# Optimization experiments

Measured on AMD Instinct MI355X. Metric: run time of the kernel, lower is better.

The kernel has to match this reference:

```python
import jax, jax.numpy as jnp
import numpy as np

B, S, D = 2, 2048, 2560
H, HKV, HD = 8, 4, 256
EPS = 1e-6
SCALING = 256 ** -0.5          # query_pre_attn_scalar ** -0.5
SOFTCAP = 4096.0               # sliding_window passed positionally into softcap slot
NEG = -1e9


def rms_norm(x, w):
    # x: [..., HD]; computed in fp32 like the torch module
    xf = x.astype(jnp.float32)
    out = xf * jax.lax.rsqrt(jnp.mean(xf * xf, axis=-1, keepdims=True) + EPS)
    return (out * (1.0 + w.astype(jnp.float32))).astype(x.dtype)


def rotate_half(x):
    x1, x2 = x[..., : HD // 2], x[..., HD // 2:]
    return jnp.concatenate((-x2, x1), axis=-1)


def apply_rope(x, cos, sin):
    # cos/sin: [B, S, HD] -> broadcast over head axis 1
    c, s = cos[:, None], sin[:, None]
    return x * c + rotate_half(x) * s


def setup_inputs() -> dict:
    key = jax.random.key(0)
    ks = jax.random.split(key, 6)
    x = jax.random.normal(ks[0], (B, S, D), dtype=jnp.float32)
    # RoPE angles (theta=10000, linear scaling factor 8)
    inv_freq = 1.0 / (10000.0 ** (np.arange(0, HD, 2, dtype=np.float32) / HD))
    pos = np.arange(S, dtype=np.float32) / 8.0
    ang = np.einsum('s,d->sd', pos, inv_freq)
    ang = np.concatenate([ang, ang], axis=-1)               # [S, HD]
    cos = jnp.asarray(np.broadcast_to(np.cos(ang), (B, S, HD)).copy())
    sin = jnp.asarray(np.broadcast_to(np.sin(ang), (B, S, HD)).copy())
    # causal additive mask [B, 1, S, S]
    causal = np.where(np.tril(np.ones((S, S), dtype=bool)), 0.0, NEG).astype(np.float32)
    mask = jnp.asarray(np.broadcast_to(causal, (B, 1, S, S)).copy())
    sc = 0.02
    q_w = jax.random.normal(ks[1], (H * HD, D), dtype=jnp.float32) * sc
    k_w = jax.random.normal(ks[2], (HKV * HD, D), dtype=jnp.float32) * sc
    v_w = jax.random.normal(ks[3], (HKV * HD, D), dtype=jnp.float32) * sc
    o_w = jax.random.normal(ks[4], (D, H * HD), dtype=jnp.float32) * sc
    qn_w = jnp.zeros((HD,), dtype=jnp.float32)
    kn_w = jnp.zeros((HD,), dtype=jnp.float32)
    return {"x": x, "cos": cos, "sin": sin, "mask": mask,
            "q_w": q_w, "k_w": k_w, "v_w": v_w, "o_w": o_w,
            "qn_w": qn_w, "kn_w": kn_w}


def reference(x, cos, sin, mask, q_w, k_w, v_w, o_w, qn_w, kn_w):
    b, s, _ = x.shape
    # projections -> [B, H(kv), S, HD]
    q = (x @ q_w.T).reshape(b, s, H, HD).transpose(0, 2, 1, 3)
    k = (x @ k_w.T).reshape(b, s, HKV, HD).transpose(0, 2, 1, 3)
    v = (x @ v_w.T).reshape(b, s, HKV, HD).transpose(0, 2, 1, 3)
    q = rms_norm(q, qn_w)
    k = rms_norm(k, kn_w)
    q = apply_rope(q, cos, sin)
    k = apply_rope(k, cos, sin)
    # GQA: repeat kv heads (interleave matches repeat_interleave on dim=1)
    rep = H // HKV
    k = jnp.repeat(k, rep, axis=1)
    v = jnp.repeat(v, rep, axis=1)
    w = jnp.einsum('bhqd,bhkd->bhqk', q, k) * SCALING
    w = jnp.tanh(w / SOFTCAP) * SOFTCAP                     # softcap (bug-faithful)
    w = w + mask[:, :, :, : k.shape[2]]
    p = jax.nn.softmax(w.astype(jnp.float32), axis=-1).astype(q.dtype)
    attn = jnp.einsum('bhqk,bhkd->bhqd', p, v)
    attn = attn.transpose(0, 2, 1, 3).reshape(b, s, H * HD)
    return attn @ o_w.T
```

## Files before the change

### kernel.cpp

```cpp
#include <hip/hip_runtime.h>
#include <hip/hip_bf16.h>

#define BB   2
#define SS   2048
#define DD   2560
#define HH   8
#define HKVV 4
#define HDD  256
#define MM   (BB*SS)
#define NQ   (HH*HDD)
#define NKV  (HKVV*HDD)
#define SCALING 0.0625f
#define SOFTCAP 4096.0f
#define CAPC    (1.0f/(3.0f*SOFTCAP*SOFTCAP))
#define M0      20.0f

typedef __attribute__((ext_vector_type(8))) short short8;
typedef __attribute__((ext_vector_type(8))) unsigned short ushort8;
typedef __attribute__((ext_vector_type(4))) unsigned short us4;
typedef __attribute__((ext_vector_type(4))) float f32x4;

__device__ __forceinline__ float bf2f(unsigned short u) {
    union { unsigned int i; float f; } v; v.i = ((unsigned int)u) << 16; return v.f;
}
__device__ __forceinline__ unsigned short f2bf(float f) {
    union { float f; unsigned int i; } v; v.f = f;
    return (unsigned short)((v.i + 0x7fffu + ((v.i >> 16) & 1u)) >> 16);
}
__device__ __forceinline__ f32x4 mfma16(short8 a, short8 b, f32x4 c) {
    return __builtin_amdgcn_mfma_f32_16x16x32_bf16(a, b, c, 0, 0, 0);
}

__device__ __forceinline__ void async_cp16(const void* g, void* l) {
    __builtin_amdgcn_global_load_lds(
        (__attribute__((address_space(1))) void*)(g),
        (__attribute__((address_space(3))) void*)(l), 16, 0, 0);
}

__device__ __forceinline__ ushort8 ld8(const unsigned short* p) { return *(const ushort8*)p; }
__device__ __forceinline__ ushort8 ld8(const float* p) {
    ushort8 r;
#pragma unroll
    for (int i = 0; i < 8; i++) r[i] = f2bf(p[i]);
    return r;
}
__device__ __forceinline__ void stc(float* p, float v)          { *p = v; }
__device__ __forceinline__ void stc(unsigned short* p, float v) { *p = f2bf(v); }
__device__ __forceinline__ void stage8(const unsigned short* src, unsigned short* lds) {
    async_cp16(src, lds);
}
__device__ __forceinline__ void stage8(const float* src, unsigned short* lds) {
    *(ushort8*)lds = ld8(src);
}

__global__ __launch_bounds__(256) void cvt_bf16(const float* __restrict__ in,
                                                unsigned short* __restrict__ out, int n4)
{
    int i = blockIdx.x * 256 + threadIdx.x;
    const int stride = gridDim.x * 256;
    for (; i < n4; i += stride) {
        float4 v = ((const float4*)in)[i];
        us4 o;
        o[0] = f2bf(v.x); o[1] = f2bf(v.y); o[2] = f2bf(v.z); o[3] = f2bf(v.w);
        ((us4*)out)[i] = o;
    }
}

__global__ __launch_bounds__(256) void cvt_w4(const float* __restrict__ s0,
                                              const float* __restrict__ s1,
                                              const float* __restrict__ s2,
                                              const float* __restrict__ s3,
                                              unsigned short* __restrict__ dst)
{
    const int y = blockIdx.y;
    const int n4q = (int)((size_t)NQ  * DD / 4);
    const int n4k = (int)((size_t)NKV * DD / 4);
    const float* src; int n4; size_t off4;
    if (y == 0)      { src = s0; n4 = n4q; off4 = 0; }
    else if (y == 1) { src = s1; n4 = n4k; off4 = (size_t)n4q; }
    else if (y == 2) { src = s2; n4 = n4k; off4 = (size_t)n4q + n4k; }
    else             { src = s3; n4 = n4q; off4 = (size_t)n4q + 2 * (size_t)n4k; }
    us4* out = (us4*)dst + off4;
    int i = blockIdx.x * 256 + threadIdx.x;
    const int stride = gridDim.x * 256;
    for (; i < n4; i += stride) {
        float4 v = ((const float4*)src)[i];
        us4 o;
        o[0] = f2bf(v.x); o[1] = f2bf(v.y); o[2] = f2bf(v.z); o[3] = f2bf(v.w);
        out[i] = o;
    }
}

template<typename TA, typename TB, typename TC, bool VT_OUT>
__global__ __launch_bounds__(256) void gemm_k(const TA* __restrict__ A,
                                              const TB* __restrict__ Bm,
                                              TC* __restrict__ C,
                                              int M, int N, int K)
{
    __shared__ __align__(16) unsigned short As[128][32];
    __shared__ __align__(16) unsigned short Bs[128][32];

    const int tid  = threadIdx.x;
    const int bm   = blockIdx.x, bn = blockIdx.y;
    const int wave = tid >> 6, lane = tid & 63;
    const int quad = lane >> 4, lm = lane & 15;
    const int wm = (wave >> 1) * 64, wn = (wave & 1) * 64;

    f32x4 acc[4][4];
#pragma unroll
    for (int i = 0; i < 4; i++)
#pragma unroll
        for (int j = 0; j < 4; j++) acc[i][j] = (f32x4)0.0f;

    unsigned short* AsF = &As[0][0];
    unsigned short* BsF = &Bs[0][0];
    const int grow = tid >> 2;
    const int gcol = (tid & 3) * 8;
    const TA* Ab = A  + (size_t)(bm * 128) * K;
    const TB* Bb = Bm + (size_t)(bn * 128) * K;

    for (int k0 = 0; k0 < K; k0 += 32) {
        stage8(&Ab[(size_t)(grow     ) * K + k0 + gcol], AsF + tid * 8);
        stage8(&Ab[(size_t)(grow + 64) * K + k0 + gcol], AsF + 2048 + tid * 8);
        stage8(&Bb[(size_t)(grow     ) * K + k0 + gcol], BsF + tid * 8);
        stage8(&Bb[(size_t)(grow + 64) * K + k0 + gcol], BsF + 2048 + tid * 8);
        __syncthreads();

        short8 af[4], bf[4];
#pragma unroll
        for (int t = 0; t < 4; t++) af[t] = *(const short8*)&As[wm + t * 16 + lm][quad * 8];
#pragma unroll
        for (int t = 0; t < 4; t++) bf[t] = *(const short8*)&Bs[wn + t * 16 + lm][quad * 8];
#pragma unroll
        for (int i = 0; i < 4; i++)
#pragma unroll
            for (int j = 0; j < 4; j++)
                acc[i][j] = mfma16(af[i], bf[j], acc[i][j]);
        __syncthreads();
    }

#pragma unroll
    for (int i = 0; i < 4; i++)
#pragma unroll
        for (int j = 0; j < 4; j++) {
            if constexpr (VT_OUT) {
                int row0 = bm * 128 + wm + i * 16 + quad * 4;
                int col  = bn * 128 + wn + j * 16 + lm;
                int b    = row0 >> 11, s0 = row0 & (SS - 1);
                int kvh  = col >> 8,   d  = col & (HDD - 1);
                us4 pk;
#pragma unroll
                for (int r = 0; r < 4; r++) pk[r] = f2bf(acc[i][j][r]);
                *(us4*)&C[(((size_t)b * HKVV + kvh) * HDD + d) * SS + s0] = pk;
            } else {
#pragma unroll
                for (int r = 0; r < 4; r++) {
                    int row = bm * 128 + wm + i * 16 + quad * 4 + r;
                    int col = bn * 128 + wn + j * 16 + lm;
                    stc(&C[(size_t)row * N + col], acc[i][j][r]);
                }
            }
        }
}

__global__ __launch_bounds__(512, 2) void gemm_qkv256(const unsigned short* __restrict__ A,
                                                      const unsigned short* __restrict__ Bm,
                                                      unsigned short* __restrict__ Qo,
                                                      unsigned short* __restrict__ Ko,
                                                      unsigned short* __restrict__ Vo,
                                                      int K)
{
    __shared__ __align__(16) unsigned short Asm[2][256 * 64];
    __shared__ __align__(16) unsigned short Bsm[2][256 * 64];

    const int tid  = threadIdx.x;
    const int wid  = tid >> 6, lane = tid & 63;
    const int quad = lane >> 4, lm = lane & 15;
    const int wr   = wid >> 2, wc = wid & 3;
    const int bm   = blockIdx.x, bn = blockIdx.y;

    f32x4 acc[8][4];
#pragma unroll
    for (int i = 0; i < 8; i++)
#pragma unroll
        for (int j = 0; j < 4; j++) acc[i][j] = (f32x4)0.0f;

    const unsigned short* Ab = A  + (size_t)(bm * 256) * K;
    const unsigned short* Bb = Bm + (size_t)(bn * 256) * K;

    auto STAGE = [&](int buf, int k0) {
#pragma unroll
        for (int p = 0; p < 4; p++) {
            const int slot = p * 512 + tid;
            const int row = slot >> 3, ch = slot & 7;
            async_cp16(&Ab[(size_t)row * K + k0 + ((ch ^ (row & 7)) * 8)],
                       &Asm[buf][slot * 8]);
        }
#pragma unroll
        for (int p = 0; p < 4; p++) {
            const int slot = p * 512 + tid;
            const int row = slot >> 3, ch = slot & 7;
            async_cp16(&Bb[(size_t)row * K + k0 + ((ch ^ (row & 7)) * 8)],
                       &Bsm[buf][slot * 8]);
        }
    };

#define LOAD_A(MH)                                                                \
    _Pragma("unroll")                                                             \
    for (int mi = 0; mi < 4; mi++) {                                              \
        const int arow = wr * 128 + ((MH) * 4 + mi) * 16 + lm;                    \
        _Pragma("unroll")                                                         \
        for (int ks = 0; ks < 2; ks++)                                            \
            a_[mi][ks] = *(const short8*)&Asm[cur][arow * 64 +                    \
                            (((ks * 4 + quad) ^ (arow & 7)) * 8)];                \
    }
#define LOAD_B(NH)                                                                \
    _Pragma("unroll")                                                             \
    for (int ni = 0; ni < 2; ni++) {                                              \
        const int brow = wc * 64 + ((NH) * 2 + ni) * 16 + lm;                     \
        _Pragma("unroll")                                                         \
        for (int ks = 0; ks < 2; ks++)                                            \
            b_[ni][ks] = *(const short8*)&Bsm[cur][brow * 64 +                    \
                            (((ks * 4 + quad) ^ (brow & 7)) * 8)];                \
    }
#define MFMA_PH(MH, NH)                                                           \
    asm volatile("s_waitcnt lgkmcnt(0)" ::: "memory");                            \
    __builtin_amdgcn_sched_barrier(0);                                            \
    __builtin_amdgcn_s_setprio(1);                                                \
    _Pragma("unroll")                                                             \
    for (int mi = 0; mi < 4; mi++)                                                \
        _Pragma("unroll")                                                         \
        for (int ni = 0; ni < 2; ni++)                                            \
            _Pragma("unroll")                                                     \
            for (int ks = 0; ks < 2; ks++)                                        \
                acc[(MH) * 4 + mi][(NH) * 2 + ni] =                               \
                    mfma16(a_[mi][ks], b_[ni][ks],                                \
                           acc[(MH) * 4 + mi][(NH) * 2 + ni]);                    \
    __builtin_amdgcn_s_setprio(0);                                                \
    __builtin_amdgcn_sched_barrier(0);

    const int NT = K >> 6;
    STAGE(0, 0);
    int cur = 0;

    for (int t = 0; t < NT; t++) {
        if (t + 1 < NT) {
            STAGE(cur ^ 1, (t + 1) * 64);
            asm volatile("s_waitcnt vmcnt(8)" ::: "memory");
        } else {
            asm volatile("s_waitcnt vmcnt(0)" ::: "memory");
        }
        __builtin_amdgcn_s_barrier();
        __builtin_amdgcn_sched_barrier(0);

        short8 a_[4][2], b_[2][2];
        LOAD_A(0) LOAD_B(0) MFMA_PH(0, 0)
        LOAD_B(1)           MFMA_PH(0, 1)
        LOAD_A(1)           MFMA_PH(1, 1)
        LOAD_B(0)           MFMA_PH(1, 0)

        __builtin_amdgcn_s_barrier();
        __builtin_amdgcn_sched_barrier(0);
        cur ^= 1;
    }
#undef LOAD_A
#undef LOAD_B
#undef MFMA_PH

    if (bn < 8) {
#pragma unroll
        for (int m = 0; m < 8; m++)
#pragma unroll
            for (int n = 0; n < 4; n++) {
                const int row0 = bm * 256 + wr * 128 + m * 16 + quad * 4;
                const int colg = bn * 256 + wc * 64 + n * 16 + lm;
#pragma unroll
                for (int r = 0; r < 4; r++)
                    Qo[(size_t)(row0 + r) * NQ + colg] = f2bf(acc[m][n][r]);
            }
    } else if (bn < 12) {
#pragma unroll
        for (int m = 0; m < 8; m++)
#pragma unroll
            for (int n = 0; n < 4; n++) {
                const int row0 = bm * 256 + wr * 128 + m * 16 + quad * 4;
                const int ck   = bn * 256 + wc * 64 + n * 16 + lm - 2048;
#pragma unroll
                for (int r = 0; r < 4; r++)
                    Ko[(size_t)(row0 + r) * NKV + ck] = f2bf(acc[m][n][r]);
            }
    } else {
#pragma unroll
        for (int m = 0; m < 8; m++)
#pragma unroll
            for (int n = 0; n < 4; n++) {
                const int row0 = bm * 256 + wr * 128 + m * 16 + quad * 4;
                const int cv   = bn * 256 + wc * 64 + n * 16 + lm - 3072;
                const int b = row0 >> 11, s0 = row0 & (SS - 1);
                const int kvh = cv >> 8, d = cv & (HDD - 1);
                us4 pk;
#pragma unroll
                for (int r = 0; r < 4; r++) pk[r] = f2bf(acc[m][n][r]);
                *(us4*)&Vo[(((size_t)b * HKVV + kvh) * HDD + d) * SS + s0] = pk;
            }
    }
}

template<typename TA>
__global__ __launch_bounds__(256) void gemm_qkv(const TA* __restrict__ A,
                                                const unsigned short* __restrict__ Bm,
                                                unsigned short* __restrict__ Qo,
                                                unsigned short* __restrict__ Ko,
                                                unsigned short* __restrict__ Vo,
                                                int K)
{
    __shared__ __align__(16) unsigned short As[128][32];
    __shared__ __align__(16) unsigned short Bs[128][32];

    const int tid  = threadIdx.x;
    const int bm   = blockIdx.x, bn = blockIdx.y;
    const int wave = tid >> 6, lane = tid & 63;
    const int quad = lane >> 4, lm = lane & 15;
    const int wm = (wave >> 1) * 64, wn = (wave & 1) * 64;

    f32x4 acc[4][4];
#pragma unroll
    for (int i = 0; i < 4; i++)
#pragma unroll
        for (int j = 0; j < 4; j++) acc[i][j] = (f32x4)0.0f;

    unsigned short* AsF = &As[0][0];
    unsigned short* BsF = &Bs[0][0];
    const int grow = tid >> 2;
    const int gcol = (tid & 3) * 8;
    const TA* Ab = A  + (size_t)(bm * 128) * K;
    const unsigned short* Bb = Bm + (size_t)(bn * 128) * K;

    for (int k0 = 0; k0 < K; k0 += 32) {
        stage8(&Ab[(size_t)(grow     ) * K + k0 + gcol], AsF + tid * 8);
        stage8(&Ab[(size_t)(grow + 64) * K + k0 + gcol], AsF + 2048 + tid * 8);
        stage8(&Bb[(size_t)(grow     ) * K + k0 + gcol], BsF + tid * 8);
        stage8(&Bb[(size_t)(grow + 64) * K + k0 + gcol], BsF + 2048 + tid * 8);
        __syncthreads();

        short8 af[4], bf[4];
#pragma unroll
        for (int t = 0; t < 4; t++) af[t] = *(const short8*)&As[wm + t * 16 + lm][quad * 8];
#pragma unroll
        for (int t = 0; t < 4; t++) bf[t] = *(const short8*)&Bs[wn + t * 16 + lm][quad * 8];
#pragma unroll
        for (int i = 0; i < 4; i++)
#pragma unroll
            for (int j = 0; j < 4; j++)
                acc[i][j] = mfma16(af[i], bf[j], acc[i][j]);
        __syncthreads();
    }

#pragma unroll
    for (int i = 0; i < 4; i++)
#pragma unroll
        for (int j = 0; j < 4; j++) {
            const int row0 = bm * 128 + wm + i * 16 + quad * 4;
            const int col  = bn * 128 + wn + j * 16 + lm;
            if (col < 2048) {
#pragma unroll
                for (int r = 0; r < 4; r++)
                    Qo[(size_t)(row0 + r) * NQ + col] = f2bf(acc[i][j][r]);
            } else if (col < 3072) {
                const int ck = col - 2048;
#pragma unroll
                for (int r = 0; r < 4; r++)
                    Ko[(size_t)(row0 + r) * NKV + ck] = f2bf(acc[i][j][r]);
            } else {
                const int cv = col - 3072;
                const int b = row0 >> 11, s0 = row0 & (SS - 1);
                const int kvh = cv >> 8, d = cv & (HDD - 1);
                us4 pk;
#pragma unroll
                for (int r = 0; r < 4; r++) pk[r] = f2bf(acc[i][j][r]);
                *(us4*)&Vo[(((size_t)b * HKVV + kvh) * HDD + d) * SS + s0] = pk;
            }
        }
}

__global__ __launch_bounds__(256) void norm_rope2(unsigned short* __restrict__ Qx,
                                                  unsigned short* __restrict__ Kx,
                                                  const float* __restrict__ qnw,
                                                  const float* __restrict__ knw,
                                                  const float* __restrict__ cosb,
                                                  const float* __restrict__ sinb)
{
    const int bs = blockIdx.x;
    const int y  = blockIdx.y;
    const int t  = threadIdx.x;
    unsigned short* X; const float* nw; int nheads, h;
    if (y < HH) { X = Qx; nw = qnw; nheads = HH;   h = y; }
    else        { X = Kx; nw = knw; nheads = HKVV; h = y - HH; }

    __shared__ float xs[256];
    __shared__ float red[4];

    const size_t base = ((size_t)bs * nheads + h) * HDD;
    float v = bf2f(X[base + t]);
    xs[t] = v;

    float p = v * v;
#pragma unroll
    for (int off = 32; off >= 1; off >>= 1) p += __shfl_xor(p, off);
    if ((t & 63) == 0) red[t >> 6] = p;
    __syncthreads();
    float sum = red[0] + red[1] + red[2] + red[3];
    float rs  = rsqrtf(sum * (1.0f / HDD) + 1e-6f);

    const int pt = (t + 128) & 255;
    float w1 = 1.0f + nw[t];
    float w2 = 1.0f + nw[pt];
    float normed  = v * rs * w1;
    float partner = xs[pt] * rs * w2;
    float rot = (t < 128) ? -partner : partner;
    float c = cosb[(size_t)bs * HDD + t];
    float s = sinb[(size_t)bs * HDD + t];
    X[base + t] = f2bf(normed * c + rot * s);
}

__global__ __launch_bounds__(256) void norm_rope(unsigned short* __restrict__ X,
                                                 const float* __restrict__ nw,
                                                 const float* __restrict__ cosb,
                                                 const float* __restrict__ sinb,
                                                 int nheads)
{
    const int bs = blockIdx.x;
    const int h  = blockIdx.y;
    const int t  = threadIdx.x;

    __shared__ float xs[256];
    __shared__ float red[4];

    const size_t base = ((size_t)bs * nheads + h) * HDD;
    float v = bf2f(X[base + t]);
    xs[t] = v;

    float p = v * v;
#pragma unroll
    for (int off = 32; off >= 1; off >>= 1) p += __shfl_xor(p, off);
    if ((t & 63) == 0) red[t >> 6] = p;
    __syncthreads();
    float sum = red[0] + red[1] + red[2] + red[3];
    float rs  = rsqrtf(sum * (1.0f / HDD) + 1e-6f);

    const int pt = (t + 128) & 255;
    float w1 = 1.0f + nw[t];
    float w2 = 1.0f + nw[pt];
    float normed  = v * rs * w1;
    float partner = xs[pt] * rs * w2;
    float rot = (t < 128) ? -partner : partner;
    float c = cosb[(size_t)bs * HDD + t];
    float s = sinb[(size_t)bs * HDD + t];
    X[base + t] = f2bf(normed * c + rot * s);
}

__device__ const unsigned char unit_tbl[48] = {
    62, 124, 125, 120, 121,
    58, 116, 117, 112, 113,
    54, 108, 109, 104, 105,
    50, 100, 101,  96,  97,
    46,  92,  93,  88,  89,
    42,  84,  85,  80,  81,
    38,  76,  77,  72,  73,
    34,  68,  69,  64,  65,
    30,  26,  22,  18,  14, 10, 6, 2
};

__global__ __launch_bounds__(256) void attn_split(const unsigned short* __restrict__ Q,
                                                  const unsigned short* __restrict__ K,
                                                  const unsigned short* __restrict__ VT,
                                                  unsigned short* __restrict__ O,
                                                  float* __restrict__ Opart,
                                                  float* __restrict__ lpart)
{
    const int tid = threadIdx.x, w = tid >> 6, lane = tid & 63;
    const int quad = lane >> 4, lm = lane & 15;
    const int hb = blockIdx.x;
    const int h = hb & 7, b = hb >> 3, kvh = h >> 1;

    const unsigned int u = unit_tbl[blockIdx.y];
    const int qb = u >> 2;
    const bool single = (u & 2) != 0;
    const int half = u & 1;
    const int q0 = qb * 64;
    const int T  = 2 * (qb + 1);
    const int t_lo = (!single && half) ? (qb + 1) : 0;
    const int t_hi = single ? T : (half ? T : (qb + 1));

    __shared__ __align__(16) unsigned short Ks[2][32 * 256];
    __shared__ __align__(16) unsigned short Vt[256 * 32];
    __shared__ __align__(16) unsigned short Ps[4 * 512];

    const unsigned short* Qb = Q + (((size_t)b * SS + q0 + w * 16 + lm) * HH + h) * HDD;
    short8 qf[8];
#pragma unroll
    for (int c = 0; c < 8; c++) qf[c] = *(const short8*)&Qb[c * 32 + quad * 8];

    const unsigned short* Kb = K  + (size_t)b * SS * NKV + (size_t)kvh * HDD;
    const unsigned short* Vb = VT + ((size_t)b * HKVV + kvh) * HDD * (size_t)SS;

    f32x4 o_acc[16];
#pragma unroll
    for (int i = 0; i < 16; i++) o_acc[i] = (f32x4)0.0f;
    float l_r[4] = {0.f, 0.f, 0.f, 0.f};

    const int mylo = q0 + w * 16;
    const int row  = mylo + quad * 4;

    auto STAGE_K = [&](int bi, int k0) {
#pragma unroll
        for (int p = 0; p < 4; p++) {
            const int slot = p * 256 + tid;
            const int krow = slot >> 5, kc = slot & 31;
            async_cp16(&Kb[(size_t)(k0 + krow) * NKV + ((kc ^ (krow & 7)) * 8)],
                       &Ks[bi][slot * 8]);
        }
    };
    auto STAGE_V = [&](int k0) {
#pragma unroll
        for (int p = 0; p < 4; p++) {
            const int slot = p * 256 + tid;
            const int vd = slot >> 2, vc = slot & 3;
            async_cp16(&Vb[(size_t)vd * SS + k0 + ((vc ^ ((vd >> 1) & 3)) * 8)],
                       &Vt[slot * 8]);
        }
    };

    STAGE_K(0, t_lo * 32);
    STAGE_V(t_lo * 32);
    int cur = 0;

    for (int t = t_lo; t < t_hi; t++) {
        const int k0 = t * 32;
        const bool more = (t + 1 < t_hi);

        if (more) {
            STAGE_K(cur ^ 1, k0 + 32);
            asm volatile("s_waitcnt vmcnt(8)" ::: "memory");
        } else {
            asm volatile("s_waitcnt vmcnt(4)" ::: "memory");
        }
        __builtin_amdgcn_s_barrier();
        __builtin_amdgcn_sched_barrier(0);

        short8 pf;
        if (k0 <= mylo + 15) {
            f32x4 sa0 = (f32x4)0.0f, sa1 = (f32x4)0.0f;
            __builtin_amdgcn_s_setprio(1);
#pragma unroll
            for (int c = 0; c < 8; c++) {
                const int cs = (((c * 4 + quad) ^ (lm & 7))) * 8;
                short8 kf0 = *(const short8*)&Ks[cur][lm * 256 + cs];
                short8 kf1 = *(const short8*)&Ks[cur][(16 + lm) * 256 + cs];
                sa0 = mfma16(qf[c], kf0, sa0);
                sa1 = mfma16(qf[c], kf1, sa1);
            }
            __builtin_amdgcn_s_setprio(0);

            const bool msk = (k0 + 31 > mylo);
            float pe[2][4];
#pragma unroll
            for (int t2 = 0; t2 < 2; t2++) {
                const int key = k0 + t2 * 16 + lm;
#pragma unroll
                for (int r = 0; r < 4; r++) {
                    float s = (t2 ? sa1[r] : sa0[r]) * SCALING;
                    s = s - s * s * s * CAPC;
                    float e = __expf(s - M0);
                    if (msk && key > row + r) e = 0.0f;
                    pe[t2][r] = e;
                    l_r[r] += e;
                }
            }

#pragma unroll
            for (int t2 = 0; t2 < 2; t2++)
#pragma unroll
                for (int r = 0; r < 4; r++) {
                    const int g = (t2 * 2 + (lm >> 3)) ^ r ^ quad;
                    Ps[w * 512 + (quad * 4 + r) * 32 + g * 8 + (lm & 7)] = f2bf(pe[t2][r]);
                }
            asm volatile("s_waitcnt lgkmcnt(0)" ::: "memory");
            __builtin_amdgcn_sched_barrier(0);
            const int gr = quad ^ (lm & 3) ^ (lm >> 2);
            pf = *(const short8*)&Ps[w * 512 + lm * 32 + gr * 8];
        }

        if (more) asm volatile("s_waitcnt vmcnt(4)" ::: "memory");
        else      asm volatile("s_waitcnt vmcnt(0)" ::: "memory");
        __builtin_amdgcn_s_barrier();
        __builtin_amdgcn_sched_barrier(0);

        if (k0 <= mylo + 15) {
            __builtin_amdgcn_s_setprio(1);
#pragma unroll
            for (int nt = 0; nt < 16; nt++) {
                short8 vf = *(const short8*)&Vt[(nt * 16 + lm) * 32
                                                + ((quad ^ ((lm >> 1) & 3)) * 8)];
                o_acc[nt] = mfma16(pf, vf, o_acc[nt]);
            }
            __builtin_amdgcn_s_setprio(0);
        }

        __builtin_amdgcn_sched_barrier(0);
        __builtin_amdgcn_s_barrier();
        __builtin_amdgcn_sched_barrier(0);
        if (more) STAGE_V(k0 + 32);
        cur ^= 1;
    }

#pragma unroll
    for (int off = 1; off < 16; off <<= 1)
#pragma unroll
        for (int r = 0; r < 4; r++) l_r[r] += __shfl_xor(l_r[r], off);

    if (single) {
#pragma unroll
        for (int r = 0; r < 4; r++) {
            float inv = 1.0f / l_r[r];
            unsigned short* Ob = O + ((size_t)b * SS + row + r) * NQ + h * HDD;
#pragma unroll
            for (int nt = 0; nt < 16; nt++)
                Ob[nt * 16 + lm] = f2bf(o_acc[nt][r] * inv);
        }
    } else {
        const int slot = (((b * HH + h) * 16 + (qb - 16)) << 1) | half;
        float* Ob = Opart + ((size_t)slot * 64 + w * 16 + quad * 4) * 256;
#pragma unroll
        for (int r = 0; r < 4; r++) {
            if (lm == 0) lpart[slot * 64 + w * 16 + quad * 4 + r] = l_r[r];
#pragma unroll
            for (int nt = 0; nt < 16; nt++)
                Ob[(size_t)r * 256 + nt * 16 + lm] = o_acc[nt][r];
        }
    }
}

__global__ __launch_bounds__(256) void attn_reduce(const float* __restrict__ Op,
                                                   const float* __restrict__ lp,
                                                   unsigned short* __restrict__ ATT)
{
    const int sp  = blockIdx.x >> 4;
    const int wr0 = (blockIdx.x & 15) * 4;
    const int r   = threadIdx.x >> 6;
    const int c0  = (threadIdx.x & 63) * 4;
    const int wrow = wr0 + r;
    const int qbm = sp & 15, h = (sp >> 4) & 7, b = sp >> 7;

    const size_t base0 = ((size_t)(sp * 2) * 64 + wrow) * 256;
    const size_t base1 = base0 + (size_t)64 * 256;
    float4 a = *(const float4*)&Op[base0 + c0];
    float4 d = *(const float4*)&Op[base1 + c0];
    float l = lp[sp * 2 * 64 + wrow] + lp[(sp * 2 + 1) * 64 + wrow];
    float inv = 1.0f / l;
    us4 o;
    o[0] = f2bf((a.x + d.x) * inv); o[1] = f2bf((a.y + d.y) * inv);
    o[2] = f2bf((a.z + d.z) * inv); o[3] = f2bf((a.w + d.w) * inv);
    const int srow = (16 + qbm) * 64 + wrow;
    *(us4*)&ATT[(((size_t)b * SS + srow) * HH + h) * HDD + c0] = o;
}

__global__ __launch_bounds__(256) void attn_kernel(const unsigned short* __restrict__ Q,
                                                   const unsigned short* __restrict__ K,
                                                   const unsigned short* __restrict__ VT,
                                                   unsigned short* __restrict__ O)
{
    const int tid = threadIdx.x, w = tid >> 6, lane = tid & 63;
    const int quad = lane >> 4, lm = lane & 15;
    const int h = blockIdx.y, b = blockIdx.z, kvh = h >> 1;

    const int bx = blockIdx.x;
    const int qb = (bx & 1) ? (31 - (bx >> 1)) : (bx >> 1);
    const int q0 = qb * 64;
    const int T  = 2 * (qb + 1);

    __shared__ __align__(16) unsigned short Ks[2][32 * 256];
    __shared__ __align__(16) unsigned short Vt[2][256 * 32];
    __shared__ __align__(16) unsigned short Ps[4 * 512];

    const unsigned short* Qb = Q + (((size_t)b * SS + q0 + w * 16 + lm) * HH + h) * HDD;
    short8 qf[8];
#pragma unroll
    for (int c = 0; c < 8; c++) qf[c] = *(const short8*)&Qb[c * 32 + quad * 8];

    const unsigned short* Kb = K  + (size_t)b * SS * NKV + (size_t)kvh * HDD;
    const unsigned short* Vb = VT + ((size_t)b * HKVV + kvh) * HDD * (size_t)SS;

    f32x4 o_acc[16];
#pragma unroll
    for (int i = 0; i < 16; i++) o_acc[i] = (f32x4)0.0f;
    float l_r[4] = {0.f, 0.f, 0.f, 0.f};

    const int mylo = q0 + w * 16;
    const int row  = mylo + quad * 4;

    auto STAGE = [&](int bi, int k0) {
#pragma unroll
        for (int p = 0; p < 4; p++) {
            const int slot = p * 256 + tid;
            const int krow = slot >> 5, kc = slot & 31;
            async_cp16(&Kb[(size_t)(k0 + krow) * NKV + ((kc ^ (krow & 7)) * 8)],
                       &Ks[bi][slot * 8]);
            const int vd = slot >> 2, vc = slot & 3;
            async_cp16(&Vb[(size_t)vd * SS + k0 + ((vc ^ ((vd >> 1) & 3)) * 8)],
                       &Vt[bi][slot * 8]);
        }
    };

    STAGE(0, 0);
    int cur = 0;

    for (int t = 0; t < T; t++) {
        const int k0 = t * 32;

        if (t + 1 < T) {
            STAGE(cur ^ 1, k0 + 32);
            asm volatile("s_waitcnt vmcnt(8)" ::: "memory");
        } else {
            asm volatile("s_waitcnt vmcnt(0)" ::: "memory");
        }
        __builtin_amdgcn_s_barrier();
        __builtin_amdgcn_sched_barrier(0);

        if (k0 <= mylo + 15) {
            f32x4 sa0 = (f32x4)0.0f, sa1 = (f32x4)0.0f;
            __builtin_amdgcn_s_setprio(1);
#pragma unroll
            for (int c = 0; c < 8; c++) {
                const int cs = (((c * 4 + quad) ^ (lm & 7))) * 8;
                short8 kf0 = *(const short8*)&Ks[cur][lm * 256 + cs];
                short8 kf1 = *(const short8*)&Ks[cur][(16 + lm) * 256 + cs];
                sa0 = mfma16(qf[c], kf0, sa0);
                sa1 = mfma16(qf[c], kf1, sa1);
            }
            __builtin_amdgcn_s_setprio(0);

            const bool msk = (k0 + 31 > mylo);
            float pe[2][4];
#pragma unroll
            for (int t2 = 0; t2 < 2; t2++) {
                const int key = k0 + t2 * 16 + lm;
#pragma unroll
                for (int r = 0; r < 4; r++) {
                    float s = (t2 ? sa1[r] : sa0[r]) * SCALING;
                    s = s - s * s * s * CAPC;
                    float e = __expf(s - M0);
                    if (msk && key > row + r) e = 0.0f;
                    pe[t2][r] = e;
                    l_r[r] += e;
                }
            }

#pragma unroll
            for (int t2 = 0; t2 < 2; t2++)
#pragma unroll
                for (int r = 0; r < 4; r++) {
                    const int g = (t2 * 2 + (lm >> 3)) ^ r ^ quad;
                    Ps[w * 512 + (quad * 4 + r) * 32 + g * 8 + (lm & 7)] = f2bf(pe[t2][r]);
                }
            asm volatile("s_waitcnt lgkmcnt(0)" ::: "memory");
            __builtin_amdgcn_sched_barrier(0);
            const int gr = quad ^ (lm & 3) ^ (lm >> 2);
            short8 pf = *(const short8*)&Ps[w * 512 + lm * 32 + gr * 8];

            __builtin_amdgcn_s_setprio(1);
#pragma unroll
            for (int nt = 0; nt < 16; nt++) {
                short8 vf = *(const short8*)&Vt[cur][(nt * 16 + lm) * 32
                                                    + ((quad ^ ((lm >> 1) & 3)) * 8)];
                o_acc[nt] = mfma16(pf, vf, o_acc[nt]);
            }
            __builtin_amdgcn_s_setprio(0);
        }

        __builtin_amdgcn_sched_barrier(0);
        __builtin_amdgcn_s_barrier();
        __builtin_amdgcn_sched_barrier(0);
        cur ^= 1;
    }

#pragma unroll
    for (int off = 1; off < 16; off <<= 1)
#pragma unroll
        for (int r = 0; r < 4; r++) l_r[r] += __shfl_xor(l_r[r], off);
#pragma unroll
    for (int r = 0; r < 4; r++) {
        float inv = 1.0f / l_r[r];
        unsigned short* Ob = O + ((size_t)b * SS + row + r) * NQ + h * HDD;
#pragma unroll
        for (int nt = 0; nt < 16; nt++)
            Ob[nt * 16 + lm] = f2bf(o_acc[nt][r] * inv);
    }
}

extern "C" void kernel_launch(void* const* d_in, const int* in_sizes, int n_in,
                              void* d_out, int out_size, void* d_ws, size_t ws_size,
                              hipStream_t stream)
{
    const float* x    = (const float*)d_in[0];
    const float* cosb = (const float*)d_in[1];
    const float* sinb = (const float*)d_in[2];
    const float* q_w  = (const float*)d_in[4];
    const float* k_w  = (const float*)d_in[5];
    const float* v_w  = (const float*)d_in[6];
    const float* o_w  = (const float*)d_in[7];
    const float* qn_w = (const float*)d_in[8];
    const float* kn_w = (const float*)d_in[9];
    float* out = (float*)d_out;

    const size_t sz_xb = (size_t)MM * DD;
    const size_t sz_wq = (size_t)NQ * DD;
    const size_t sz_wk = (size_t)NKV * DD;
    const size_t sz_q  = (size_t)MM * NQ;
    const size_t sz_k  = (size_t)MM * NKV;

    const size_t needA = (sz_xb + 2 * sz_wq + 2 * sz_wk + sz_q + 2 * sz_k) * 2;
    const size_t needB = (2 * sz_wq + 2 * sz_wk + sz_q + 2 * sz_k) * 2;

    if (ws_size >= needA) {
        unsigned short* xb  = (unsigned short*)d_ws;
        unsigned short* wqb = xb  + sz_xb;
        unsigned short* wkb = wqb + sz_wq;
        unsigned short* wvb = wkb + sz_wk;
        unsigned short* wob = wvb + sz_wk;
        unsigned short* Qw  = wob + sz_wq;
        unsigned short* Kw  = Qw  + sz_q;
        unsigned short* VTw = Kw  + sz_k;
        float* Opart = (float*)d_ws;
        float* lpart = Opart + (size_t)512 * 64 * 256;
        unsigned short* ATT = Qw;

        cvt_bf16<<<2048, 256, 0, stream>>>(x, xb, (int)(sz_xb / 4));
        cvt_w4<<<dim3(512, 4), 256, 0, stream>>>(q_w, k_w, v_w, o_w, wqb);

        gemm_qkv256<<<dim3(MM/256, 4096/256), 512, 0, stream>>>(xb, wqb, Qw, Kw, VTw, DD);

        norm_rope2<<<dim3(MM, HH + HKVV), 256, 0, stream>>>(Qw, Kw, qn_w, kn_w, cosb, sinb);

        attn_split<<<dim3(16, 48), 256, 0, stream>>>(Qw, Kw, VTw, ATT, Opart, lpart);
        attn_reduce<<<4096, 256, 0, stream>>>(Opart, lpart, ATT);

        gemm_k<unsigned short, unsigned short, float, false>
            <<<dim3(MM/128, DD/128), 256, 0, stream>>>(ATT, wob, out, MM, DD, NQ);
    } else if (ws_size >= needB) {
        unsigned short* wqb = (unsigned short*)d_ws;
        unsigned short* wkb = wqb + sz_wq;
        unsigned short* wvb = wkb + sz_wk;
        unsigned short* wob = wvb + sz_wk;
        unsigned short* Qw  = wob + sz_wq;
        unsigned short* Kw  = Qw  + sz_q;
        unsigned short* VTw = Kw  + sz_k;
        unsigned short* ATT = wqb;

        cvt_w4<<<dim3(512, 4), 256, 0, stream>>>(q_w, k_w, v_w, o_w, wqb);

        gemm_qkv<float>
            <<<dim3(MM/128, 4096/128), 256, 0, stream>>>(x, wqb, Qw, Kw, VTw, DD);

        norm_rope2<<<dim3(MM, HH + HKVV), 256, 0, stream>>>(Qw, Kw, qn_w, kn_w, cosb, sinb);

        attn_kernel<<<dim3(32, HH, BB), 256, 0, stream>>>(Qw, Kw, VTw, ATT);

        gemm_k<unsigned short, unsigned short, float, false>
            <<<dim3(MM/128, DD/128), 256, 0, stream>>>(ATT, wob, out, MM, DD, NQ);
    } else {
        unsigned short* Qw  = (unsigned short*)d_ws;
        unsigned short* Kw  = Qw  + sz_q;
        unsigned short* VTw = Kw  + sz_k;
        unsigned short* ATT = VTw + sz_k;

        gemm_k<float, float, unsigned short, false>
            <<<dim3(MM/128, NQ /128), 256, 0, stream>>>(x, q_w, Qw,  MM, NQ,  DD);
        gemm_k<float, float, unsigned short, false>
            <<<dim3(MM/128, NKV/128), 256, 0, stream>>>(x, k_w, Kw,  MM, NKV, DD);
        gemm_k<float, float, unsigned short, true>
            <<<dim3(MM/128, NKV/128), 256, 0, stream>>>(x, v_w, VTw, MM, NKV, DD);

        norm_rope<<<dim3(MM, HH),   256, 0, stream>>>(Qw, qn_w, cosb, sinb, HH);
        norm_rope<<<dim3(MM, HKVV), 256, 0, stream>>>(Kw, kn_w, cosb, sinb, HKVV);

        attn_kernel<<<dim3(32, HH, BB), 256, 0, stream>>>(Qw, Kw, VTw, ATT);

        gemm_k<unsigned short, float, float, false>
            <<<dim3(MM/128, DD/128), 256, 0, stream>>>(ATT, o_w, out, MM, DD, NQ);
    }
}
```

Measured before the change: 446.8 us.

## Interleave async global loads with MFMA phases and reuse 256-tile GEMM for output projection

The 256x256-tile GEMM now issues its next-stage async copies in pairs interleaved between the MFMA phases instead of all at once before the barrier, and waits with a smaller vmcnt so loads overlap compute. The kernel is templated with a route that writes fp32 output directly, and the output projection switches from the 128-tile gemm_k to this 256-tile kernel. The aim is to hide global-load latency and raise per-block reuse on the O projection. In exchange, the O GEMM gets only 16x10=160 blocks, which may underfill the GPU's compute units, and the new vmcnt accounting relies on exact counts of outstanding copies.

```diff
diff --git a/kernel.cpp b/kernel.cpp
--- a/kernel.cpp
+++ b/kernel.cpp
@@ -163,12 +163,14 @@
         }
 }
 
-__global__ __launch_bounds__(512, 2) void gemm_qkv256(const unsigned short* __restrict__ A,
-                                                      const unsigned short* __restrict__ Bm,
-                                                      unsigned short* __restrict__ Qo,
-                                                      unsigned short* __restrict__ Ko,
-                                                      unsigned short* __restrict__ Vo,
-                                                      int K)
+template<int ROUTE>
+__global__ __launch_bounds__(512, 2) void gemm256(const unsigned short* __restrict__ A,
+                                                  const unsigned short* __restrict__ Bm,
+                                                  unsigned short* __restrict__ Qo,
+                                                  unsigned short* __restrict__ Ko,
+                                                  unsigned short* __restrict__ Vo,
+                                                  float* __restrict__ Cf,
+                                                  int K)
 {
     __shared__ __align__(16) unsigned short Asm[2][256 * 64];
     __shared__ __align__(16) unsigned short Bsm[2][256 * 64];
@@ -188,21 +190,15 @@
     const unsigned short* Ab = A  + (size_t)(bm * 256) * K;
     const unsigned short* Bb = Bm + (size_t)(bn * 256) * K;
 
-    auto STAGE = [&](int buf, int k0) {
-#pragma unroll
-        for (int p = 0; p < 4; p++) {
-            const int slot = p * 512 + tid;
-            const int row = slot >> 3, ch = slot & 7;
+    auto STAGE1 = [&](int buf, int k0, int p) {
+        const int slot = (p & 3) * 512 + tid;
+        const int row = slot >> 3, ch = slot & 7;
+        if (p < 4)
             async_cp16(&Ab[(size_t)row * K + k0 + ((ch ^ (row & 7)) * 8)],
                        &Asm[buf][slot * 8]);
-        }
-#pragma unroll
-        for (int p = 0; p < 4; p++) {
-            const int slot = p * 512 + tid;
-            const int row = slot >> 3, ch = slot & 7;
+        else
             async_cp16(&Bb[(size_t)row * K + k0 + ((ch ^ (row & 7)) * 8)],
                        &Bsm[buf][slot * 8]);
-        }
     };
 
 #define LOAD_A(MH)                                                                \
@@ -240,13 +236,17 @@
     __builtin_amdgcn_sched_barrier(0);
 
     const int NT = K >> 6;
-    STAGE(0, 0);
+#pragma unroll
+    for (int p = 0; p < 8; p++) STAGE1(0, 0, p);
     int cur = 0;
 
     for (int t = 0; t < NT; t++) {
-        if (t + 1 < NT) {
-            STAGE(cur ^ 1, (t + 1) * 64);
-            asm volatile("s_waitcnt vmcnt(8)" ::: "memory");
+        const bool more = (t + 1 < NT);
+        const int nb = cur ^ 1, nk = (t + 1) * 64;
+
+        if (more) {
+            STAGE1(nb, nk, 0); STAGE1(nb, nk, 1);
+            asm volatile("s_waitcnt vmcnt(2)" ::: "memory");
         } else {
             asm volatile("s_waitcnt vmcnt(0)" ::: "memory");
         }
@@ -255,8 +255,11 @@
 
         short8 a_[4][2], b_[2][2];
         LOAD_A(0) LOAD_B(0) MFMA_PH(0, 0)
+        if (more) { STAGE1(nb, nk, 2); STAGE1(nb, nk, 3); }
         LOAD_B(1)           MFMA_PH(0, 1)
+        if (more) { STAGE1(nb, nk, 4); STAGE1(nb, nk, 5); }
         LOAD_A(1)           MFMA_PH(1, 1)
+        if (more) { STAGE1(nb, nk, 6); STAGE1(nb, nk, 7); }
         LOAD_B(0)           MFMA_PH(1, 0)
 
         __builtin_amdgcn_s_barrier();
@@ -267,7 +270,18 @@
 #undef LOAD_B
 #undef MFMA_PH
 
-    if (bn < 8) {
+    if constexpr (ROUTE == 1) {
+#pragma unroll
+        for (int m = 0; m < 8; m++)
+#pragma unroll
+            for (int n = 0; n < 4; n++) {
+                const int row0 = bm * 256 + wr * 128 + m * 16 + quad * 4;
+                const int col  = bn * 256 + wc * 64 + n * 16 + lm;
+#pragma unroll
+                for (int r = 0; r < 4; r++)
+                    Cf[(size_t)(row0 + r) * DD + col] = acc[m][n][r];
+            }
+    } else if (bn < 8) {
 #pragma unroll
         for (int m = 0; m < 8; m++)
 #pragma unroll
@@ -838,15 +852,16 @@
         cvt_bf16<<<2048, 256, 0, stream>>>(x, xb, (int)(sz_xb / 4));
         cvt_w4<<<dim3(512, 4), 256, 0, stream>>>(q_w, k_w, v_w, o_w, wqb);
 
-        gemm_qkv256<<<dim3(MM/256, 4096/256), 512, 0, stream>>>(xb, wqb, Qw, Kw, VTw, DD);
+        gemm256<0><<<dim3(MM/256, 4096/256), 512, 0, stream>>>(
+            xb, wqb, Qw, Kw, VTw, nullptr, DD);
 
         norm_rope2<<<dim3(MM, HH + HKVV), 256, 0, stream>>>(Qw, Kw, qn_w, kn_w, cosb, sinb);
 
         attn_split<<<dim3(16, 48), 256, 0, stream>>>(Qw, Kw, VTw, ATT, Opart, lpart);
         attn_reduce<<<4096, 256, 0, stream>>>(Opart, lpart, ATT);
 
-        gemm_k<unsigned short, unsigned short, float, false>
-            <<<dim3(MM/128, DD/128), 256, 0, stream>>>(ATT, wob, out, MM, DD, NQ);
+        gemm256<1><<<dim3(MM/256, DD/256), 512, 0, stream>>>(
+            ATT, wob, nullptr, nullptr, nullptr, out, NQ);
     } else if (ws_size >= needB) {
         unsigned short* wqb = (unsigned short*)d_ws;
         unsigned short* wkb = wqb + sz_wq;
```

After: 471.1 us. 1.05x slower.
